# Optimization experiments

Measured on AMD Instinct MI355X. Metric: run time of the kernel, lower is better.

## Reference

```python
import jax, jax.numpy as jnp
import numpy as np

D = 1024          # feature dim (x_dim)
C = 32            # n classes (way)
SHOTS = 32
N_SUP = C * SHOTS
Q = 1024
REG = 0.5         # reg_param


def setup_inputs() -> dict:
    key = jax.random.key(0)
    ks = jax.random.split(key, 5)
    support_x = jax.random.normal(ks[0], (N_SUP, D), dtype=jnp.float32)
    query_x = jax.random.normal(ks[1], (Q, D), dtype=jnp.float32)
    labels_idx = (jnp.arange(N_SUP, dtype=jnp.int32) % C)  # every class present, equal shots
    m = jax.random.normal(ks[2], (1, D), dtype=jnp.float32) * 0.01
    kappa = jnp.float32(0.1)
    nu = jnp.float32(D)
    triu_diag = jnp.ones((D,), dtype=jnp.float32)
    triu_lower = jnp.eye(D, dtype=jnp.float32) + 0.01 * jax.random.normal(ks[3], (D, D), dtype=jnp.float32)
    return {"support_x": support_x, "query_x": query_x, "labels_idx": labels_idx,
            "m": m, "kappa": kappa, "nu": nu,
            "triu_diag": triu_diag, "triu_lower": triu_lower}


def _metaqda_fb(support_x, query_x, labels_idx, m, kappa, nu, triu_diag, triu_lower):
    onehot = jax.nn.one_hot(labels_idx, C, dtype=support_x.dtype)      # [N, C]
    Nj = jnp.sum(onehot, axis=0)                                       # [C]
    kappa_ = jnp.abs(kappa) + 1e-6
    nu_ = jnp.maximum(nu, jnp.float32(D - 1 + 1e-6))

    # Cholesky-factor prior scatter matrix: L @ L^T
    lower_mask = jnp.tril(jnp.ones((D, D), dtype=support_x.dtype), k=-1)
    L = jnp.diag(jnp.abs(triu_diag)) + triu_lower * lower_mask
    prior_S = L @ L.T                                                  # [D, D]

    # per-class sums (replaces python loop of rank-1 outer products with GEMMs)
    sum_x = onehot.T @ support_x                                       # [C, D]
    mean_x = sum_x / Nj[:, None]
    # sum_n x x^T per class: contract through [N,C,D] intermediate
    SXX = jnp.einsum('nc,nd,ne->cde', onehot, support_x, support_x)    # [C, D, D]

    kN = kappa_ + Nj                                                   # [C]
    mu = (kappa_ / kN)[:, None] * m + (Nj / kN)[:, None] * mean_x      # [C, D]

    mm = m.T @ m                                                       # [D, D]  (self_outer of [1,D])
    mumu = jnp.einsum('cd,ce->cde', mu, mu)                            # [C, D, D]
    S = prior_S[None] + SXX + kappa_ * mm[None] - kN[:, None, None] * mumu

    scale = (kN + 1.0) / ((nu_ + Nj - D + 1.0) * kN)                   # [C]
    sigma = S * scale[:, None, None]                                   # [C, D, D]

    sigma_inv = (1.0 - REG) * jnp.linalg.inv(sigma) + REG * jnp.eye(D, dtype=sigma.dtype)

    common = nu_ + Nj + 1.0 - D                                        # [C]
    _, logdet = jnp.linalg.slogdet(sigma)
    bias = (jax.lax.lgamma(0.5 * (common + D)) - jax.lax.lgamma(0.5 * common)
            - 0.5 * D * jnp.log(common) - 0.5 * logdet)                # [C]

    diff = query_x[:, None, :] - mu[None, :, :]                        # [Q, C, D]
    dist = jnp.einsum('qcd,cde,qce->qc', diff, sigma_inv, diff)        # [Q, C]
    preds = bias[None, :] - 0.5 * (common + D)[None, :] * jnp.log1p(dist / common[None, :])
    return preds


def reference(support_x, query_x, labels_idx, m, kappa, nu, triu_diag, triu_lower):
    return _metaqda_fb(support_x, query_x, labels_idx, m, kappa, nu, triu_diag, triu_lower)
```

## Files before the change

### kernel.cpp

```cpp
#include <hip/hip_runtime.h>
#include <math.h>

#define Dk 1024
#define Ck 32
#define Nk 1024
#define Qk 1024
#define REGP 0.5f
#define NB 64
#define NROWSV (Qk + Nk + Ck + 1)

#define CO_KAPPA 0
#define CO_NU    1
#define CO_NJ    2
#define CO_KN    34
#define CO_SCALE 66
#define CO_COMMON 98
#define CO_COEF  130
#define CO_BIASA 162
#define CO_BIASF 200

#define O_P    0u
#define O_W    2162688u
#define O_T    3211264u
#define O_MU   3473408u
#define O_QM   3506176u
#define O_MB   3538944u
#define O_MI   3578112u
#define O_QNY  3617280u
#define O_QNO  3618304u
#define O_MUN  3619328u
#define O_GMM  3619360u
#define O_EX   3619392u
#define O_CONS 3619408u
#define O_CIDX 3619664u
#define O_YH   3652432u
#define O_YM   4733776u
#define O_YL   5815120u
#define O_WH   6896464u
#define O_WM   7420752u
#define O_WL   7945040u
#define O_OH   8469328u
#define O_OM   9550672u
#define O_OL   10632016u

#define WS_DECL \
    float* P     = Wbuf + O_P;    (void)P; \
    float* W     = Wbuf + O_W;    (void)W; \
    float* Tb    = Wbuf + O_T;    (void)Tb; \
    float* QM    = Wbuf + O_QM;   (void)QM; \
    float* Mbuf  = Wbuf + O_MB;   (void)Mbuf; \
    float* Minv  = Wbuf + O_MI;   (void)Minv; \
    float* qny   = Wbuf + O_QNY;  (void)qny; \
    float* qno   = Wbuf + O_QNO;  (void)qno; \
    float* mun2o = Wbuf + O_MUN;  (void)mun2o; \
    float* gmm   = Wbuf + O_GMM;  (void)gmm; \
    float* extraf= Wbuf + O_EX;   (void)extraf; \
    float* cons  = Wbuf + O_CONS; (void)cons; \
    int*   cidx  = (int*)(Wbuf + O_CIDX); (void)cidx; \
    ushort* sYh = (ushort*)(Wbuf + O_YH); (void)sYh; \
    ushort* sYm = (ushort*)(Wbuf + O_YM); (void)sYm; \
    ushort* sYl = (ushort*)(Wbuf + O_YL); (void)sYl; \
    ushort* sWh = (ushort*)(Wbuf + O_WH); (void)sWh; \
    ushort* sWm = (ushort*)(Wbuf + O_WM); (void)sWm; \
    ushort* sWl = (ushort*)(Wbuf + O_WL); (void)sWl; \
    ushort* sOh = (ushort*)(Wbuf + O_OH); (void)sOh; \
    ushort* sOm = (ushort*)(Wbuf + O_OM); (void)sOm; \
    ushort* sOl = (ushort*)(Wbuf + O_OL); (void)sOl;

typedef __attribute__((ext_vector_type(8))) __bf16 bf16x8;
typedef __attribute__((ext_vector_type(4))) float f32x4;

#define MFMA(a, b, c) __builtin_amdgcn_mfma_f32_16x16x32_bf16(a, b, c, 0, 0, 0)

__device__ __forceinline__ ushort f2bf(float x) {
    unsigned u = __float_as_uint(x);
    return (ushort)((u + 0x7FFFu + ((u >> 16) & 1u)) >> 16);
}
__device__ __forceinline__ float bf2f(ushort h) {
    return __uint_as_float(((unsigned)h) << 16);
}
__device__ __forceinline__ void split1(float x, ushort& h, ushort& m, ushort& l) {
    h = f2bf(x);
    float r1 = x - bf2f(h);
    m = f2bf(r1);
    l = f2bf(r1 - bf2f(m));
}
__device__ __forceinline__ void split_store4(ushort* ph, ushort* pm, ushort* pl,
                                             size_t o, float4 v) {
    float vv[4] = {v.x, v.y, v.z, v.w};
    ushort4 H, M, L;
    ushort* Hp = (ushort*)&H; ushort* Mp = (ushort*)&M; ushort* Lp = (ushort*)&L;
#pragma unroll
    for (int c = 0; c < 4; ++c) split1(vv[c], Hp[c], Mp[c], Lp[c]);
    *(ushort4*)(ph + o) = H;
    *(ushort4*)(pm + o) = M;
    *(ushort4*)(pl + o) = L;
}

__device__ __forceinline__ float wave_red(float s) {
#pragma unroll
    for (int o = 32; o > 0; o >>= 1) s += __shfl_down(s, o, 64);
    return s;
}

#define LDSB3(c, r, k8) ((c) * 5120 + (r) * 40 + (k8))
#define LDS_BUF 15360
#define LDS_HW3 30720

__device__ __forceinline__ void b_fetch3(bf16x8* rb,
                                         const ushort* Bh, const ushort* Bm, const ushort* Bl,
                                         int bRow0, int kcol, int t) {
#pragma unroll
    for (int u = 0; u < 6; ++u) {
        int comp = u >> 1;
        int idx = ((u & 1) << 8) + t;
        int row = idx >> 2, kg = idx & 3;
        const ushort* Bs = (comp == 0) ? Bh : ((comp == 1) ? Bm : Bl);
        rb[u] = *(const bf16x8*)(Bs + (size_t)(bRow0 + row) * 1024 + kcol + kg * 8);
    }
}
__device__ __forceinline__ void b_store3(ushort* ldsb, const bf16x8* rb, int t) {
#pragma unroll
    for (int u = 0; u < 6; ++u) {
        int comp = u >> 1;
        int idx = ((u & 1) << 8) + t;
        int row = idx >> 2, kg = idx & 3;
        *(bf16x8*)(ldsb + LDSB3(comp, row, kg * 8)) = rb[u];
    }
}
__device__ __forceinline__ void a_fetch3(bf16x8 af[4][3],
                                         const ushort* Ah, const ushort* Am, const ushort* Al,
                                         int arowT, int aRowMax, int kcol, int lk) {
    bf16x8 z = {};
#pragma unroll
    for (int rf = 0; rf < 4; ++rf) {
        int gr = arowT + rf * 16;
        bool ok = gr < aRowMax;
#pragma unroll
        for (int c = 0; c < 3; ++c) {
            const ushort* As = (c == 0) ? Ah : ((c == 1) ? Am : Al);
            af[rf][c] = ok ? *(const bf16x8*)(As + (size_t)gr * 1024 + kcol + lk * 8) : z;
        }
    }
}

__device__ __forceinline__ void tile_compute3(const ushort* ldsb, f32x4 acc[4][4],
                                              bf16x8 af[4][3], int bcol0, int lr, int lk) {
#pragma unroll
    for (int cf = 0; cf < 4; ++cf) {
        int brow = bcol0 + cf * 16 + lr;
        bf16x8 bh = *(const bf16x8*)(ldsb + LDSB3(0, brow, lk * 8));
        bf16x8 bm = *(const bf16x8*)(ldsb + LDSB3(1, brow, lk * 8));
        bf16x8 bl = *(const bf16x8*)(ldsb + LDSB3(2, brow, lk * 8));
#pragma unroll
        for (int rf = 0; rf < 4; ++rf) {
            f32x4 a = acc[rf][cf];
            a = MFMA(af[rf][0], bh, a);
            a = MFMA(af[rf][0], bm, a);
            a = MFMA(af[rf][1], bh, a);
            a = MFMA(af[rf][0], bl, a);
            a = MFMA(af[rf][2], bh, a);
            a = MFMA(af[rf][1], bm, a);
            acc[rf][cf] = a;
        }
    }
}

__device__ __forceinline__ void tile_gemm3(
    ushort* lds, f32x4 acc[4][4],
    const ushort* Ah, const ushort* Am, const ushort* Al, int aRow0, int aRowMax,
    const ushort* Bh, const ushort* Bm, const ushort* Bl, int bRow0,
    int kbase, int ksteps, int t)
{
    const int w = t >> 6, lr = t & 15, lk = (t >> 4) & 3;
    const int arowT = aRow0 + (w >> 1) * 64 + lr;
    const int bcol0 = (w & 1) * 64;
    bf16x8 rb[6], afc[4][3], afn[4][3];
    b_fetch3(rb, Bh, Bm, Bl, bRow0, kbase * 32, t);
    a_fetch3(afc, Ah, Am, Al, arowT, aRowMax, kbase * 32, lk);
    b_store3(lds, rb, t);
    __syncthreads();
    for (int kt = 0; kt < ksteps; ++kt) {
        ushort* cur = lds + (kt & 1) * LDS_BUF;
        ushort* nxt = lds + ((kt + 1) & 1) * LDS_BUF;
        if (kt + 1 < ksteps) {
            b_fetch3(rb, Bh, Bm, Bl, bRow0, (kbase + kt + 1) * 32, t);
            a_fetch3(afn, Ah, Am, Al, arowT, aRowMax, (kbase + kt + 1) * 32, lk);
        }
        tile_compute3(cur, acc, afc, bcol0, lr, lk);
        if (kt + 1 < ksteps) {
            b_store3(nxt, rb, t);
#pragma unroll
            for (int rf = 0; rf < 4; ++rf)
#pragma unroll
                for (int c = 0; c < 3; ++c) afc[rf][c] = afn[rf][c];
        }
        __syncthreads();
    }
}

__device__ __forceinline__ void fetch4(float4* reg, const float* src, int ld,
                                       int rowbase, int rowmax, int colbase, int t) {
#pragma unroll
    for (int u = 0; u < 4; ++u) {
        int slot = t + u * 256;
        int r = slot >> 4, c4 = slot & 15;
        int gr = rowbase + r;
        reg[u] = (gr < rowmax) ? *(const float4*)(src + (size_t)gr * ld + colbase + c4 * 4)
                               : make_float4(0.f, 0.f, 0.f, 0.f);
    }
}
__device__ __forceinline__ void stT(float* dst, const float4* reg, int t) {
#pragma unroll
    for (int u = 0; u < 4; ++u) {
        int slot = t + u * 256;
        int r = slot >> 4, c4 = slot & 15;
        dst[(c4 * 4 + 0) * 68 + r] = reg[u].x;
        dst[(c4 * 4 + 1) * 68 + r] = reg[u].y;
        dst[(c4 * 4 + 2) * 68 + r] = reg[u].z;
        dst[(c4 * 4 + 3) * 68 + r] = reg[u].w;
    }
}
__device__ __forceinline__ void stN(float* dst, const float4* reg, int t) {
#pragma unroll
    for (int u = 0; u < 4; ++u) {
        int slot = t + u * 256;
        int r = slot >> 4, c4 = slot & 15;
        *(float4*)(dst + r * 68 + c4 * 4) = reg[u];
    }
}
__device__ __forceinline__ void gemm16(const float* At, const float* Bt,
                                       float acc[4][4], int tx, int ty) {
#pragma unroll 4
    for (int kk = 0; kk < NB; ++kk) {
        float4 a = *(const float4*)(At + kk * 68 + ty * 4);
        float4 b = *(const float4*)(Bt + kk * 68 + tx * 4);
        float av[4] = {a.x, a.y, a.z, a.w};
        float bv[4] = {b.x, b.y, b.z, b.w};
#pragma unroll
        for (int r = 0; r < 4; ++r)
#pragma unroll
            for (int s = 0; s < 4; ++s) acc[r][s] += av[r] * bv[s];
    }
}
__device__ __forceinline__ void mm_task(
    const float* aSrc, int aLd, int aRow, int aRowMax, int aCol, int aRowStep, int aColStep,
    const float* bSrc, int bLd, int bRow, int bRowMax, int bCol, int bRowStep, int bColStep,
    bool bTrans, int k0, int k1,
    float acc[4][4], float* smA, float* smB, int t, int tx, int ty)
{
    float4 ra[4], rb[4];
    fetch4(ra, aSrc, aLd, aRow + k0 * aRowStep, aRowMax, aCol + k0 * aColStep, t);
    fetch4(rb, bSrc, bLd, bRow + k0 * bRowStep, bRowMax, bCol + k0 * bColStep, t);
    stT(smA, ra, t);
    if (bTrans) stT(smB, rb, t); else stN(smB, rb, t);
    __syncthreads();
    for (int kt = k0; kt < k1; ++kt) {
        if (kt + 1 < k1) {
            fetch4(ra, aSrc, aLd, aRow + (kt + 1) * aRowStep, aRowMax, aCol + (kt + 1) * aColStep, t);
            fetch4(rb, bSrc, bLd, bRow + (kt + 1) * bRowStep, bRowMax, bCol + (kt + 1) * bColStep, t);
        }
        gemm16(smA, smB, acc, tx, ty);
        __syncthreads();
        if (kt + 1 < k1) {
            stT(smA, ra, t);
            if (bTrans) stT(smB, rb, t); else stN(smB, rb, t);
        }
        __syncthreads();
    }
}

__global__ __launch_bounds__(256) void k_p0(const float* qx, const int* labels,
                                            const float* mvec, const float* kappa,
                                            const float* nu, const float* td,
                                            const float* tl, float* Wbuf) {
    __shared__ __align__(16) float smem[9216];
    float* sX  = smem + 8704;
    WS_DECL
    float* Yo32 = Wbuf;
    const int t = threadIdx.x;
    const int lane = t & 63, wv = t >> 6;
    const int tau = blockIdx.x;

    if (tau == 0) {
        int* scnt = (int*)sX;
        if (t < Ck) scnt[t] = 0;
        __syncthreads();
        for (int n = t; n < Nk; n += 256) {
            int l = labels[n];
            int pos = atomicAdd(&scnt[l], 1);
            cidx[l * Nk + pos] = n;
        }
        __syncthreads();
        if (t < Ck) {
            float kap = fabsf(kappa[0]) + 1e-6f;
            float nu_ = fmaxf(nu[0], (float)(Dk - 1) + 1e-6f);
            float Njf = (float)scnt[t];
            float kN = kap + Njf;
            if (t == 0) { cons[CO_KAPPA] = kap; cons[CO_NU] = nu_; }
            cons[CO_NJ + t] = Njf;
            cons[CO_KN + t] = kN;
            cons[CO_SCALE + t] = (kN + 1.0f) / ((nu_ + Njf - (float)Dk + 1.0f) * kN);
            float common = nu_ + Njf + 1.0f - (float)Dk;
            cons[CO_COMMON + t] = common;
            cons[CO_COEF + t] = 0.5f * (common + (float)Dk);
            cons[CO_BIASA + t] = lgammaf(0.5f * (common + (float)Dk)) - lgammaf(0.5f * common)
                                 - 0.5f * (float)Dk * logf(common);
        }
    } else if (tau == 1) {
        float s = 0.f;
        for (int i = t; i < Dk; i += 256) s += logf(fabsf(td[i]));
        s = wave_red(s);
        if (lane == 0) sX[wv] = s;
        __syncthreads();
        if (t == 0) extraf[0] = 2.f * (sX[0] + sX[1] + sX[2] + sX[3]);
    } else if (tau < 18) {
        int b0 = (tau - 2) * NB;
        for (int idx = t; idx < 64 * 64; idx += 256) {
            int m = idx >> 6, i = idx & 63;
            smem[i * 72 + m] = (m > i) ? tl[(size_t)(b0 + m) * Dk + b0 + i] : 0.f;
        }
        if (t < 64) smem[4608 + t] = 1.f / fabsf(td[b0 + t]);
        __syncthreads();
        if (t < 64) {
            const int j = t;
            float r[64];
#pragma unroll
            for (int m = 0; m < 64; ++m) r[m] = (m == j) ? 1.f : 0.f;
#pragma unroll
            for (int i = 0; i < 64; ++i) {
                float x = r[i] * smem[4608 + i];
                r[i] = x;
#pragma unroll
                for (int g = (i >> 2); g < 16; ++g) {
                    float4 lt = *(const float4*)&smem[i * 72 + g * 4];
                    r[g * 4 + 0] -= lt.x * x;
                    r[g * 4 + 1] -= lt.y * x;
                    r[g * 4 + 2] -= lt.z * x;
                    r[g * 4 + 3] -= lt.w * x;
                }
            }
#pragma unroll
            for (int i = 0; i < 64; ++i)
                W[(size_t)(b0 + i) * Dk + b0 + j] = r[i];
        }
    } else if (tau < 21) {
        int base = (tau - 18) * 13056;
        for (int i = t; i < 13056 && base + i < 39168; i += 256) Mbuf[base + i] = 0.f;
    } else if (tau == 21) {
        if (t < 32) { mun2o[t] = 0.f; gmm[t] = 0.f; }
        for (int i = t; i < 8192; i += 256)
            ((float4*)QM)[i] = make_float4(0, 0, 0, 0);
        if (t < 256) ((float4*)qny)[t] = make_float4(0, 0, 0, 0);
    } else if (tau < 86) {
        int rbase = (tau - 22) * 16;
        for (int j = wv; j < 16; j += 4) {
            const float* row = qx + (size_t)(rbase + j) * Dk;
            float s = 0.f;
            for (int d = lane; d < Dk; d += 64) { float v = row[d]; s += v * v; }
            s = wave_red(s);
            if (lane == 0) qno[rbase + j] = s;
        }
    } else if (tau < 150) {
        int rbase = (tau - 86) * 16;
        for (int j = 0; j < 16; ++j) {
            int r = rbase + j;
            float4 v = ((const float4*)(qx + (size_t)r * Dk))[t];
            split_store4(sYh, sYm, sYl, (size_t)r * 1024 + (size_t)t * 4, v);
        }
    } else if (tau == 150) {
        float4 v = ((const float4*)mvec)[t];
        split_store4(sYh, sYm, sYl, (size_t)2080 * 1024 + (size_t)t * 4, v);
    } else {
        int rbase = (tau - 151) * 16;
        for (int j = 0; j < 16; ++j)
            ((float4*)(Yo32 + (size_t)(rbase + j) * 1024))[t] = make_float4(0, 0, 0, 0);
    }
}

__global__ __launch_bounds__(256) void k_p1(const float* sx, const float* mvec,
                                            const float* tl, float* Wbuf) {
    __shared__ __align__(16) float smem[8704];
    WS_DECL
    const int t = threadIdx.x;
    const int lane = t & 63, wv = t >> 6;
    const int tau = blockIdx.x;
    if (tau < 128) {
        float* sX = smem;
        int c = tau >> 2;
        int d = ((tau & 3) << 8) + t;
        int Nj = (int)cons[CO_NJ + c];
        float kap = cons[CO_KAPPA], kN = cons[CO_KN + c];
        float acc = 0.f;
        for (int s = 0; s < Nj; ++s) acc += sx[(size_t)cidx[c * Nk + s] * Dk + d];
        float muv = (kap * mvec[d] + acc) / kN;
        size_t o = (size_t)(2048 + c) * 1024 + d;
        ushort h, m_, l_;
        split1(muv, h, m_, l_);
        sYh[o] = h; sYm[o] = m_; sYl[o] = l_;
        float s2 = wave_red(muv * muv);
        if (lane == 0) sX[wv] = s2;
        __syncthreads();
        if (t == 0) atomicAdd(&mun2o[c], sX[0] + sX[1] + sX[2] + sX[3]);
    } else if (tau < 192) {
        int rbase = (tau - 128) * 16;
        for (int j = 0; j < 16; ++j) {
            int n = rbase + j;
            int srcrow = cidx[(n >> 5) * Nk + (n & 31)];
            float4 v = ((const float4*)(sx + (size_t)srcrow * Dk))[t];
            split_store4(sYh, sYm, sYl, (size_t)(1024 + n) * 1024 + (size_t)t * 4, v);
        }
    } else {
        float* smA = smem;
        float* smB = smem + 4352;
        const int tx = t & 15, ty = t >> 4;
        const int BIG = 1 << 30;
        int pb = (tau - 192) * 128;
        float acc[4][4] = {};
        mm_task(tl, Dk, pb + 64, BIG, pb, 0, NB,
                W, Dk, pb, BIG, pb, NB, 0, false, 0, 1,
                acc, smA, smB, t, tx, ty);
        {
            float4 ra[4];
            fetch4(ra, W, Dk, pb + 64, BIG, pb + 64, t);
#pragma unroll
            for (int r = 0; r < 4; ++r)
#pragma unroll
                for (int s = 0; s < 4; ++s)
                    smB[(ty * 4 + r) * 68 + tx * 4 + s] = acc[r][s];
            stT(smA, ra, t);
        }
        __syncthreads();
        float acc2[4][4] = {};
        gemm16(smA, smB, acc2, tx, ty);
        __syncthreads();
#pragma unroll
        for (int r = 0; r < 4; ++r)
#pragma unroll
            for (int s = 0; s < 4; ++s)
                W[(size_t)(pb + 64 + ty * 4 + r) * Dk + pb + tx * 4 + s] = -acc2[r][s];
    }
}

__global__ __launch_bounds__(256) void k_tr_a(const float* tl, float* Wbuf, int h, int ht) {
    __shared__ __align__(16) float smem[8704];
    float* smA = smem;
    float* smB = smem + 4352;
    WS_DECL
    const int t = threadIdx.x;
    const int tx = t & 15, ty = t >> 4;
    const int BIG = 1 << 30;
    int tau = blockIdx.x;
    int p = tau / (ht * ht), rr = tau % (ht * ht);
    int i = rr / ht, j = rr % ht;
    int pb = p * 2 * h;
    float acc[4][4] = {};
    mm_task(tl, Dk, pb + h + i * NB, BIG, pb, 0, NB,
            W, Dk, pb, BIG, pb + j * NB, NB, 0, false, 0, ht,
            acc, smA, smB, t, tx, ty);
    float* Tp = Tb + (size_t)p * h * h;
#pragma unroll
    for (int r = 0; r < 4; ++r)
#pragma unroll
        for (int s = 0; s < 4; ++s)
            Tp[(size_t)(i * NB + ty * 4 + r) * h + j * NB + tx * 4 + s] = acc[r][s];
}

__global__ __launch_bounds__(256) void k_tr_b(float* Wbuf, int h, int ht) {
    __shared__ __align__(16) float smem[8704];
    float* smA = smem;
    float* smB = smem + 4352;
    WS_DECL
    const int t = threadIdx.x;
    const int tx = t & 15, ty = t >> 4;
    const int BIG = 1 << 30;
    int tau = blockIdx.x;
    int p = tau / (ht * ht), rr = tau % (ht * ht);
    int i = rr / ht, j = rr % ht;
    int pb = p * 2 * h;
    const float* Tp = Tb + (size_t)p * h * h;
    float acc[4][4] = {};
    mm_task(W, Dk, pb + h + i * NB, BIG, pb + h, 0, NB,
            Tp, h, 0, BIG, j * NB, NB, 0, false, 0, ht,
            acc, smA, smB, t, tx, ty);
#pragma unroll
    for (int r = 0; r < 4; ++r)
#pragma unroll
        for (int s = 0; s < 4; ++s)
            W[(size_t)(pb + h + i * NB + ty * 4 + r) * Dk + pb + j * NB + tx * 4 + s] = -acc[r][s];
}

__global__ __launch_bounds__(256) void k_cvtw(float* Wbuf) {
    WS_DECL
    const int t = threadIdx.x;
#pragma unroll
    for (int u = 0; u < 4; ++u) {
        unsigned g = blockIdx.x * 1024u + u * 256u + t;
        int row = g >> 8, col4 = (g & 255) * 4;
        float4 v = ((const float4*)W)[g];
        if (col4 + 0 > row) v.x = 0.f;
        if (col4 + 1 > row) v.y = 0.f;
        if (col4 + 2 > row) v.z = 0.f;
        if (col4 + 3 > row) v.w = 0.f;
        split_store4(sWh, sWm, sWl, (size_t)g * 4, v);
    }
}

__global__ __launch_bounds__(256) void k_yg(float* Wbuf) {
    __shared__ __align__(16) ushort lds[LDS_HW3];
    WS_DECL
    float* Yo32 = Wbuf;
    const int t = threadIdx.x;
    int b = blockIdx.x;
    int xcd = b & 7, pos = b >> 3;
    int e = (xcd < 4) ? xcd * 43 + pos : 172 + (xcd - 4) * 42 + pos;
    int q = e / 17, rt = e % 17;
    int jt2, kc;
    if (q < 4)       { jt2 = 7; kc = q; }
    else if (q < 8)  { jt2 = 6; kc = q - 4; }
    else if (q < 11) { jt2 = 5; kc = q - 8; }
    else if (q < 14) { jt2 = 4; kc = q - 11; }
    else if (q < 16) { jt2 = 3; kc = q - 14; }
    else if (q < 18) { jt2 = 2; kc = q - 16; }
    else if (q == 18){ jt2 = 1; kc = 0; }
    else             { jt2 = 0; kc = 0; }
    int ksteps = min(8, 4 * (jt2 + 1) - kc * 8);
    f32x4 acc[4][4] = {};
    tile_gemm3(lds, acc, sYh, sYm, sYl, rt * 128, 2081,
               sWh, sWm, sWl, jt2 * 128, kc * 8, ksteps, t);
    const int w = t >> 6, lr = t & 15, lk = (t >> 4) & 3;
#pragma unroll
    for (int rf = 0; rf < 4; ++rf)
#pragma unroll
        for (int cf = 0; cf < 4; ++cf)
#pragma unroll
            for (int r = 0; r < 4; ++r) {
                int grow = rt * 128 + (w >> 1) * 64 + rf * 16 + lk * 4 + r;
                if (grow < NROWSV)
                    atomicAdd(&Yo32[(size_t)grow * 1024 + jt2 * 128 + (w & 1) * 64 + cf * 16 + lr],
                              acc[rf][cf][r]);
            }
}

__global__ __launch_bounds__(256) void k_cvto(float* Wbuf) {
    __shared__ float sred[16];
    WS_DECL
    float* Yo32 = Wbuf;
    const int t = threadIdx.x;
    const int lane = t & 63, wv = t >> 6;
    int rbase = blockIdx.x * 4;
    float4 vv[4];
#pragma unroll
    for (int j = 0; j < 4; ++j) {
        int r = rbase + j;
        float4 v = ((const float4*)(Yo32 + (size_t)r * 1024))[t];
        vv[j] = v;
        split_store4(sOh, sOm, sOl, (size_t)r * 1024 + (size_t)t * 4, v);
    }
    if (rbase < 1024) {
#pragma unroll
        for (int j = 0; j < 4; ++j) {
            float4 v = vv[j];
            float s = v.x * v.x + v.y * v.y + v.z * v.z + v.w * v.w;
            s = wave_red(s);
            if (lane == 0) sred[wv * 4 + j] = s;
        }
        __syncthreads();
        if (t < 4)
            qny[rbase + t] = sred[t] + sred[4 + t] + sred[8 + t] + sred[12 + t];
    }
    if (rbase < 1088) {
#pragma unroll
        for (int j = 0; j < 4; ++j)
            ((float4*)(Yo32 + (size_t)(rbase + j) * 1024))[t] = make_float4(0, 0, 0, 0);
    }
}

__global__ __launch_bounds__(256) void k_p4m(float* Wbuf) {
    __shared__ __align__(16) ushort lds[LDS_HW3];
    WS_DECL
    const int t = threadIdx.x;
    int b = blockIdx.x;
    int e = (b & 7) * 40 + (b >> 3);
    const int w = t >> 6, lr = t & 15, lk = (t >> 4) & 3;
    f32x4 acc[4][4] = {};
    if (e < 288) {
        int qt2 = e / 36, rem = e % 36;
        int mt = rem >> 2, kc = rem & 3;
        tile_gemm3(lds, acc, sOh, sOm, sOl, 1024 + mt * 128, 2081,
                   sOh, sOm, sOl, qt2 * 128, kc * 8, 8, t);
#pragma unroll
        for (int rf = 0; rf < 4; ++rf)
#pragma unroll
            for (int cf = 0; cf < 4; ++cf)
#pragma unroll
                for (int r = 0; r < 4; ++r) {
                    int n = mt * 128 + (w >> 1) * 64 + rf * 16 + lk * 4 + r;
                    if (n < Nk + Ck + 1)
                        atomicAdd(&P[(size_t)n * 1024 + qt2 * 128 + (w & 1) * 64 + cf * 16 + lr],
                                  acc[rf][cf][r]);
                }
    } else {
        int f = e - 288;
        int qt2 = f >> 2, kc = f & 3;
        tile_gemm3(lds, acc, sYh, sYm, sYl, 2048, 2080,
                   sYh, sYm, sYl, qt2 * 128, kc * 8, 8, t);
#pragma unroll
        for (int rf = 0; rf < 4; ++rf)
#pragma unroll
            for (int cf = 0; cf < 4; ++cf)
#pragma unroll
                for (int r = 0; r < 4; ++r) {
                    int rq = (w >> 1) * 64 + rf * 16 + lk * 4 + r;
                    if (rq < 32)
                        atomicAdd(&QM[(size_t)rq * 1024 + qt2 * 128 + (w & 1) * 64 + cf * 16 + lr],
                                  acc[rf][cf][r]);
                }
    }
}

__global__ __launch_bounds__(256) void k_gram(float* Wbuf) {
    __shared__ __align__(16) float smA[34 * 68];
    WS_DECL
    const int t = threadIdx.x;
    const int tau = blockIdx.x;
    int c = tau >> 2, kc = tau & 3;
    float accg[5];
    int iu[5], ju[5];
#pragma unroll
    for (int u = 0; u < 5; ++u) {
        int e = t + u * 256;
        iu[u] = e / 34; ju[u] = e - iu[u] * 34;
        accg[u] = 0.f;
    }
    for (int kt = kc * 4; kt < kc * 4 + 4; ++kt) {
        for (int e2 = t; e2 < 34 * NB; e2 += 256) {
            int i = e2 >> 6, k = e2 & 63;
            int yr = (i < 32) ? (Qk + c * 32 + i) : ((i == 32) ? (Qk + Nk + c) : (Qk + Nk + Ck));
            size_t o = (size_t)yr * 1024 + kt * NB + k;
            smA[i * 68 + k] = bf2f(sOh[o]) + bf2f(sOm[o]) + bf2f(sOl[o]);
        }
        __syncthreads();
#pragma unroll
        for (int u = 0; u < 5; ++u) {
            int e = t + u * 256;
            if (e < 1156) {
                float s = 0.f;
                for (int k = 0; k < NB; ++k) s += smA[iu[u] * 68 + k] * smA[ju[u] * 68 + k];
                accg[u] += s;
            }
        }
        __syncthreads();
    }
#pragma unroll
    for (int u = 0; u < 5; ++u) {
        int e = t + u * 256;
        if (e < 1156)
            atomicAdd(&Mbuf[c * 1224 + iu[u] * 36 + ju[u]], accg[u]);
    }
}

__global__ __launch_bounds__(64) void k_p5(float* Wbuf) {
    __shared__ __align__(16) float A[34 * 36];
    WS_DECL
    const int t = threadIdx.x;
    const int c = blockIdx.x;
    float kN = cons[CO_KN + c], kap = cons[CO_KAPPA];
    for (int e = t; e < 34 * 34; e += 64) {
        int i = e / 34, j = e - i * 34;
        A[i * 36 + j] = Mbuf[c * 1224 + i * 36 + j];
    }
    __syncthreads();
    if (t == 0) {
        gmm[c] = A[32 * 36 + 32];
        A[32 * 36 + 32] += -1.f / kN;
        A[33 * 36 + 33] += 1.f / kap;
    }
    if (t < 32) A[t * 36 + t] += 1.f;
    __syncthreads();
    float ldacc = 0.f;
    for (int j = 0; j < 34; ++j) {
        float piv = A[j * 36 + j];
        float pinv = 1.f / piv;
        if (t == 0) ldacc += logf(fabsf(piv));
        if (t < 34 && t != j) A[j * 36 + t] *= pinv;
        __syncthreads();
        if (t < 34) {
            if (t != j) {
                float f = A[t * 36 + j];
                float4* rowT = (float4*)(A + t * 36);
                const float4* rowJ = (const float4*)(A + j * 36);
#pragma unroll
                for (int k4 = 0; k4 < 8; ++k4) {
                    float4 rv = rowT[k4], pv = rowJ[k4];
                    rv.x -= f * pv.x; rv.y -= f * pv.y;
                    rv.z -= f * pv.z; rv.w -= f * pv.w;
                    rowT[k4] = rv;
                }
                A[t * 36 + 32] -= f * A[j * 36 + 32];
                A[t * 36 + 33] -= f * A[j * 36 + 33];
                A[t * 36 + j] = -f * pinv;
            } else {
                A[j * 36 + j] = pinv;
            }
        }
        __syncthreads();
    }
    for (int e = t; e < 34 * 34; e += 64) {
        int i = e / 34, j = e - i * 34;
        Minv[c * 1224 + i * 36 + j] = A[i * 36 + j];
    }
    if (t == 0) {
        float scale = cons[CO_SCALE + c];
        float logdet = (float)Dk * logf(scale) + extraf[0] + logf(kN) + logf(kap) + ldacc;
        cons[CO_BIASF + c] = cons[CO_BIASA + c] - 0.5f * logdet;
    }
}

__global__ __launch_bounds__(256) void k_p6(float* Wbuf, float* out) {
    __shared__ __align__(16) float smem[3904];
    float* Mi  = smem;
    float* wL  = smem + 1200;
    float* gsm = smem + 3520;
    float* red = smem + 3520 + 128;
    WS_DECL
    const int t = threadIdx.x;
    const int tau = blockIdx.x;
    int qt = tau >> 5, c = tau & 31;
    for (int e = t; e < 34 * 34; e += 256) {
        int i = e / 34, j = e - i * 34;
        Mi[i * 35 + j] = Minv[c * 1224 + i * 36 + j];
    }
    if (t < 34)
        gsm[t] = (t < 32) ? Mbuf[c * 1224 + t * 36 + 32]
                          : ((t == 32) ? gmm[c] : Mbuf[c * 1224 + 33 * 36 + 32]);
    __syncthreads();
    for (int e = t; e < 34 * NB; e += 256) {
        int i = e >> 6, qq = e & 63;
        int prow = (i < 32) ? (c * 32 + i) : ((i == 32) ? (Nk + c) : (Nk + Ck));
        wL[i * 68 + qq] = P[(size_t)prow * Qk + qt * NB + qq] - gsm[i];
    }
    __syncthreads();
    {
        int q = t & 63, part = t >> 6;
        int start = (part < 2) ? part * 9 : 18 + (part - 2) * 8;
        int cnt = (part < 2) ? 9 : 8;
        float partial = 0.f;
        for (int i = start; i < start + cnt; ++i) {
            float v = 0.f;
            for (int j = 0; j < 34; ++j) v += Mi[i * 35 + j] * wL[j * 68 + q];
            partial += v * wL[i * 68 + q];
        }
        red[part * 64 + q] = partial;
    }
    __syncthreads();
    if (t < 64) {
        int q = t;
        float quad = red[q] + red[64 + q] + red[128 + q] + red[192 + q];
        int qg = qt * NB + q;
        float w32 = wL[32 * 68 + q];
        float ydist2 = qny[qg] - 2.f * w32 - gmm[c];
        float dd = qno[qg] + mun2o[c] - 2.f * QM[(size_t)c * Qk + qg];
        float scale = cons[CO_SCALE + c], common = cons[CO_COMMON + c];
        float dist = (1.f - REGP) / scale * (ydist2 - quad) + REGP * dd;
        out[(size_t)qg * Ck + c] = cons[CO_BIASF + c] - cons[CO_COEF + c] * log1pf(dist / common);
    }
}

extern "C" void kernel_launch(void* const* d_in, const int* in_sizes, int n_in,
                              void* d_out, int out_size, void* d_ws, size_t ws_size,
                              hipStream_t stream) {
    const float* sx = (const float*)d_in[0];
    const float* qx = (const float*)d_in[1];
    const int* labels = (const int*)d_in[2];
    const float* mvec = (const float*)d_in[3];
    const float* kappa = (const float*)d_in[4];
    const float* nu = (const float*)d_in[5];
    const float* td = (const float*)d_in[6];
    const float* tl = (const float*)d_in[7];
    float* W = (float*)d_ws;
    float* out = (float*)d_out;

    hipLaunchKernelGGL(k_p0, dim3(283), dim3(256), 0, stream,
                       qx, labels, mvec, kappa, nu, td, tl, W);
    hipLaunchKernelGGL(k_p1, dim3(200), dim3(256), 0, stream, sx, mvec, tl, W);
    for (int l = 2; l <= 4; ++l) {
        int h = 32 << l, ht = h >> 6, pairs = 16 >> l;
        int nt = pairs * ht * ht;
        hipLaunchKernelGGL(k_tr_a, dim3(nt), dim3(256), 0, stream, tl, W, h, ht);
        hipLaunchKernelGGL(k_tr_b, dim3(nt), dim3(256), 0, stream, W, h, ht);
    }
    hipLaunchKernelGGL(k_cvtw, dim3(256), dim3(256), 0, stream, W);
    hipLaunchKernelGGL(k_yg, dim3(340), dim3(256), 0, stream, W);
    hipLaunchKernelGGL(k_cvto, dim3(528), dim3(256), 0, stream, W);
    hipLaunchKernelGGL(k_p4m, dim3(320), dim3(256), 0, stream, W);
    hipLaunchKernelGGL(k_gram, dim3(128), dim3(256), 0, stream, W);
    hipLaunchKernelGGL(k_p5, dim3(32), dim3(64), 0, stream, W);
    hipLaunchKernelGGL(k_p6, dim3(512), dim3(256), 0, stream, W, out);
}
```

Before: 398.5 us.

## Single-buffer GEMM LDS tile and parallelize 64x64 triangular inverse across 256 threads

The split-bf16 GEMM tile loop drops its LDS double buffer and uses one buffer with an extra barrier between compute and the store of the next tile. This halves LDS use (LDS_HW3 goes from 30720 to 15360 ushorts), which may allow more blocks per CU but serializes the LDS store behind compute. The diagonal-block triangular inverse, which used only 64 threads each holding 64 registers, now spreads rows over four wave groups of 16 rows each. Those groups exchange solved values through shared memory with a barrier per row.

New measurement: 391.1 us. Within noise of the previous version (-1.8%).

```diff
diff --git a/kernel.cpp b/kernel.cpp
--- a/kernel.cpp
+++ b/kernel.cpp
@@ -104,8 +104,7 @@
 }
 
 #define LDSB3(c, r, k8) ((c) * 5120 + (r) * 40 + (k8))
-#define LDS_BUF 15360
-#define LDS_HW3 30720
+#define LDS_HW3 15360
 
 __device__ __forceinline__ void b_fetch3(bf16x8* rb,
                                          const ushort* Bh, const ushort* Bm, const ushort* Bl,
@@ -119,13 +118,13 @@
         rb[u] = *(const bf16x8*)(Bs + (size_t)(bRow0 + row) * 1024 + kcol + kg * 8);
     }
 }
-__device__ __forceinline__ void b_store3(ushort* ldsb, const bf16x8* rb, int t) {
+__device__ __forceinline__ void b_store3(ushort* lds, const bf16x8* rb, int t) {
 #pragma unroll
     for (int u = 0; u < 6; ++u) {
         int comp = u >> 1;
         int idx = ((u & 1) << 8) + t;
         int row = idx >> 2, kg = idx & 3;
-        *(bf16x8*)(ldsb + LDSB3(comp, row, kg * 8)) = rb[u];
+        *(bf16x8*)(lds + LDSB3(comp, row, kg * 8)) = rb[u];
     }
 }
 __device__ __forceinline__ void a_fetch3(bf16x8 af[4][3],
@@ -144,14 +143,14 @@
     }
 }
 
-__device__ __forceinline__ void tile_compute3(const ushort* ldsb, f32x4 acc[4][4],
+__device__ __forceinline__ void tile_compute3(const ushort* lds, f32x4 acc[4][4],
                                               bf16x8 af[4][3], int bcol0, int lr, int lk) {
 #pragma unroll
     for (int cf = 0; cf < 4; ++cf) {
         int brow = bcol0 + cf * 16 + lr;
-        bf16x8 bh = *(const bf16x8*)(ldsb + LDSB3(0, brow, lk * 8));
-        bf16x8 bm = *(const bf16x8*)(ldsb + LDSB3(1, brow, lk * 8));
-        bf16x8 bl = *(const bf16x8*)(ldsb + LDSB3(2, brow, lk * 8));
+        bf16x8 bh = *(const bf16x8*)(lds + LDSB3(0, brow, lk * 8));
+        bf16x8 bm = *(const bf16x8*)(lds + LDSB3(1, brow, lk * 8));
+        bf16x8 bl = *(const bf16x8*)(lds + LDSB3(2, brow, lk * 8));
 #pragma unroll
         for (int rf = 0; rf < 4; ++rf) {
             f32x4 a = acc[rf][cf];
@@ -181,15 +180,14 @@
     b_store3(lds, rb, t);
     __syncthreads();
     for (int kt = 0; kt < ksteps; ++kt) {
-        ushort* cur = lds + (kt & 1) * LDS_BUF;
-        ushort* nxt = lds + ((kt + 1) & 1) * LDS_BUF;
         if (kt + 1 < ksteps) {
             b_fetch3(rb, Bh, Bm, Bl, bRow0, (kbase + kt + 1) * 32, t);
             a_fetch3(afn, Ah, Am, Al, arowT, aRowMax, (kbase + kt + 1) * 32, lk);
         }
-        tile_compute3(cur, acc, afc, bcol0, lr, lk);
+        tile_compute3(lds, acc, afc, bcol0, lr, lk);
+        __syncthreads();
         if (kt + 1 < ksteps) {
-            b_store3(nxt, rb, t);
+            b_store3(lds, rb, t);
 #pragma unroll
             for (int rf = 0; rf < 4; ++rf)
 #pragma unroll
@@ -316,34 +314,44 @@
         if (t == 0) extraf[0] = 2.f * (sX[0] + sX[1] + sX[2] + sX[3]);
     } else if (tau < 18) {
         int b0 = (tau - 2) * NB;
+        float* Ld   = smem;
+        float* dinv = smem + 4160;
+        float* bx   = smem + 4224;
+        const int j = t & 63, mg = t >> 6;
         for (int idx = t; idx < 64 * 64; idx += 256) {
             int m = idx >> 6, i = idx & 63;
-            smem[i * 72 + m] = (m > i) ? tl[(size_t)(b0 + m) * Dk + b0 + i] : 0.f;
-        }
-        if (t < 64) smem[4608 + t] = 1.f / fabsf(td[b0 + t]);
-        __syncthreads();
-        if (t < 64) {
-            const int j = t;
-            float r[64];
-#pragma unroll
-            for (int m = 0; m < 64; ++m) r[m] = (m == j) ? 1.f : 0.f;
-#pragma unroll
-            for (int i = 0; i < 64; ++i) {
-                float x = r[i] * smem[4608 + i];
-                r[i] = x;
-#pragma unroll
-                for (int g = (i >> 2); g < 16; ++g) {
-                    float4 lt = *(const float4*)&smem[i * 72 + g * 4];
-                    r[g * 4 + 0] -= lt.x * x;
-                    r[g * 4 + 1] -= lt.y * x;
-                    r[g * 4 + 2] -= lt.z * x;
-                    r[g * 4 + 3] -= lt.w * x;
+            Ld[m * 65 + i] = (m > i) ? tl[(size_t)(b0 + m) * Dk + b0 + i] : 0.f;
+        }
+        if (t < 64) dinv[t] = 1.f / fabsf(td[b0 + t]);
+        __syncthreads();
+        float x[16];
+#pragma unroll
+        for (int u = 0; u < 16; ++u) x[u] = (mg * 16 + u == j) ? 1.f : 0.f;
+        for (int ig = 0; ig < 4; ++ig) {
+            for (int ii = 0; ii < 16; ++ii) {
+                int i = ig * 16 + ii;
+                if (mg == ig) {
+                    float dv = dinv[i];
+                    float xi = 0.f;
+#pragma unroll
+                    for (int u = 0; u < 16; ++u)
+                        if (u == ii) { xi = x[u] * dv; x[u] = xi; }
+                    bx[(i & 1) * 64 + j] = xi;
+                }
+                __syncthreads();
+                float bxv = bx[(i & 1) * 64 + j];
+                if (mg >= ig) {
+#pragma unroll
+                    for (int u = 0; u < 16; ++u)
+                        if (mg * 16 + u > i)
+                            x[u] -= Ld[(mg * 16 + u) * 65 + i] * bxv;
                 }
             }
-#pragma unroll
-            for (int i = 0; i < 64; ++i)
-                W[(size_t)(b0 + i) * Dk + b0 + j] = r[i];
-        }
+        }
+        __syncthreads();
+#pragma unroll
+        for (int u = 0; u < 16; ++u)
+            W[(size_t)(b0 + mg * 16 + u) * Dk + b0 + j] = x[u];
     } else if (tau < 21) {
         int base = (tau - 18) * 13056;
         for (int i = t; i < 13056 && base + i < 39168; i += 256) Mbuf[base + i] = 0.f;
@@ -354,17 +362,17 @@
         if (t < 256) ((float4*)qny)[t] = make_float4(0, 0, 0, 0);
     } else if (tau < 86) {
         int rbase = (tau - 22) * 16;
-        for (int j = wv; j < 16; j += 4) {
-            const float* row = qx + (size_t)(rbase + j) * Dk;
+        for (int j2 = wv; j2 < 16; j2 += 4) {
+            const float* row = qx + (size_t)(rbase + j2) * Dk;
             float s = 0.f;
             for (int d = lane; d < Dk; d += 64) { float v = row[d]; s += v * v; }
             s = wave_red(s);
-            if (lane == 0) qno[rbase + j] = s;
+            if (lane == 0) qno[rbase + j2] = s;
         }
     } else if (tau < 150) {
         int rbase = (tau - 86) * 16;
-        for (int j = 0; j < 16; ++j) {
-            int r = rbase + j;
+        for (int j2 = 0; j2 < 16; ++j2) {
+            int r = rbase + j2;
             float4 v = ((const float4*)(qx + (size_t)r * Dk))[t];
             split_store4(sYh, sYm, sYl, (size_t)r * 1024 + (size_t)t * 4, v);
         }
@@ -373,8 +381,8 @@
         split_store4(sYh, sYm, sYl, (size_t)2080 * 1024 + (size_t)t * 4, v);
     } else {
         int rbase = (tau - 151) * 16;
-        for (int j = 0; j < 16; ++j)
-            ((float4*)(Yo32 + (size_t)(rbase + j) * 1024))[t] = make_float4(0, 0, 0, 0);
+        for (int j2 = 0; j2 < 16; ++j2)
+            ((float4*)(Yo32 + (size_t)(rbase + j2) * 1024))[t] = make_float4(0, 0, 0, 0);
     }
 }
 
```
